# Performance work log

Measured on AMD Instinct MI355X. Metric: run time of the kernel, lower is better.

## Reference

```python
import jax, jax.numpy as jnp
import numpy as np
from jax import lax

B, T, HID = 4, 1024, 1024
H, DK, DV = 8, 128, 128
KCONV = 4
EPS = 1e-6
KEY_DIM = H * DK          # 1024
VAL_DIM = H * DV          # 1024
CONV_DIM = 2 * KEY_DIM + VAL_DIM  # 3072


def setup_inputs() -> dict:
    key = jax.random.key(0)
    ks = jax.random.split(key, 11)
    s = 0.02
    return {
        "hidden_states": jax.random.normal(ks[0], (B, T, HID), jnp.float32),
        "qkv_w": jax.random.normal(ks[1], (CONV_DIM, HID), jnp.float32) * s,
        "z_w": jax.random.normal(ks[2], (VAL_DIM, HID), jnp.float32) * s,
        "b_w": jax.random.normal(ks[3], (H, HID), jnp.float32) * s,
        "a_w": jax.random.normal(ks[4], (H, HID), jnp.float32) * s,
        "conv_w": jax.random.normal(ks[5], (CONV_DIM, 1, KCONV), jnp.float32) * 0.2,
        "dt_bias": jnp.ones((H,), jnp.float32),
        "A_log": jnp.log(jax.random.uniform(ks[6], (H,), jnp.float32, 1e-3, 16.0)),
        "norm_w": jnp.ones((DV,), jnp.float32),
        "out_w": jax.random.normal(ks[7], (HID, VAL_DIM), jnp.float32) * s,
    }


def reference(hidden_states, qkv_w, z_w, b_w, a_w, conv_w, dt_bias, A_log, norm_w, out_w):
    b_, t_, _ = hidden_states.shape

    # qkv projection -> [B, T, CONV_DIM]
    mixed = jnp.einsum("bth,ch->btc", hidden_states, qkv_w)

    # causal depthwise conv1d over time (groups == channels, padding K-1, truncated)
    x = mixed.transpose(0, 2, 1)  # [B, C, T]
    x = lax.conv_general_dilated(
        x, conv_w, window_strides=(1,), padding=[(KCONV - 1, 0)],
        feature_group_count=CONV_DIM,
        dimension_numbers=("NCH", "OIH", "NCH"))
    mixed = x.transpose(0, 2, 1)  # [B, T, C]

    z = jnp.einsum("bth,vh->btv", hidden_states, z_w).reshape(b_, t_, H, DV)
    bb = jnp.einsum("bth,nh->btn", hidden_states, b_w)   # [B,T,H]
    aa = jnp.einsum("bth,nh->btn", hidden_states, a_w)   # [B,T,H]

    q, k, v = jnp.split(mixed, 3, axis=-1)
    q = q.reshape(b_, t_, H, DK)
    k = k.reshape(b_, t_, H, DK)
    v = v.reshape(b_, t_, H, DV)

    beta = jax.nn.sigmoid(bb)                                  # [B,T,H]
    g = -jnp.exp(A_log) * jax.nn.softplus(aa + dt_bias)        # [B,T,H]
    alpha = jnp.exp(g)                                         # per-step decay

    # gated delta rule recurrence, time-major scan
    def step(S, inp):
        q_t, k_t, v_t, beta_t, alpha_t = inp  # [B,H,dk],[B,H,dk],[B,H,dv],[B,H],[B,H]
        S = S * alpha_t[..., None, None]                       # decay state
        kv = jnp.einsum("bhk,bhkv->bhv", k_t, S)              # retrieved memory
        S = S + jnp.einsum("bhk,bhv->bhkv", k_t, (v_t - kv) * beta_t[..., None])
        o_t = jnp.einsum("bhk,bhkv->bhv", q_t, S)
        return S, o_t

    qt = q.transpose(1, 0, 2, 3)
    kt = k.transpose(1, 0, 2, 3)
    vt = v.transpose(1, 0, 2, 3)
    bt = beta.transpose(1, 0, 2)
    at = alpha.transpose(1, 0, 2)
    S0 = jnp.zeros((b_, H, DK, DV), hidden_states.dtype)
    _, o = lax.scan(step, S0, (qt, kt, vt, bt, at))            # o: [T,B,H,dv]
    o = o.transpose(1, 0, 2, 3)                                # [B,T,H,dv]

    # gated RMSNorm: rmsnorm(o) * weight * silu(z)
    var = jnp.mean(jnp.square(o), axis=-1, keepdims=True)
    o = o * lax.rsqrt(var + EPS) * norm_w
    o = o * (z * jax.nn.sigmoid(z))

    out = jnp.einsum("btv,hv->bth", o.reshape(b_, t_, VAL_DIM), out_w)
    return out
```

## Files before the change

### kernel.cpp

```cpp
#include <hip/hip_runtime.h>

#define B_ 4
#define T_ 1024
#define HID_ 1024
#define H_ 8
#define CONV_DIM_ 3072
#define MROWS (B_*T_)

typedef __bf16 bf16x8 __attribute__((ext_vector_type(8)));
typedef float f32x4 __attribute__((ext_vector_type(4)));

#define MFMA16(a,b,c) __builtin_amdgcn_mfma_f32_16x16x32_bf16((a),(b),(c),0,0,0)

static __device__ __forceinline__ unsigned short f2bf(float f) {
  unsigned u = __float_as_uint(f);
  unsigned r = u + 0x7fffu + ((u >> 16) & 1u);
  return (unsigned short)(r >> 16);
}
static __device__ __forceinline__ float bfu2f(unsigned short v) {
  return __uint_as_float(((unsigned)v) << 16);
}
static __device__ __forceinline__ float4 recon4(ushort4 h, ushort4 l) {
  float4 r;
  r.x = bfu2f(h.x) + bfu2f(l.x);
  r.y = bfu2f(h.y) + bfu2f(l.y);
  r.z = bfu2f(h.z) + bfu2f(l.z);
  r.w = bfu2f(h.w) + bfu2f(l.w);
  return r;
}

static __device__ __forceinline__ void gld16(void* lds, const void* g) {
  __builtin_amdgcn_global_load_lds(
      (const __attribute__((address_space(1))) unsigned int*)g,
      (__attribute__((address_space(3))) unsigned int*)lds, 16, 0, 0);
}

__global__ __launch_bounds__(256) void f2bf_kernel(
    const float* __restrict__ src, unsigned short* __restrict__ dst, int n) {
  int i = (blockIdx.x * 256 + threadIdx.x) * 4;
  if (i >= n) return;
  float4 v = *(const float4*)(src + i);
  ushort4 o;
  o.x = f2bf(v.x); o.y = f2bf(v.y); o.z = f2bf(v.z); o.w = f2bf(v.w);
  *(ushort4*)(dst + i) = o;
}

__global__ __launch_bounds__(256) void f2bf_split_kernel(
    const float* __restrict__ src, unsigned short* __restrict__ hi,
    unsigned short* __restrict__ lo, int n) {
  int i = (blockIdx.x * 256 + threadIdx.x) * 4;
  if (i >= n) return;
  float4 v = *(const float4*)(src + i);
  ushort4 h, l;
  h.x = f2bf(v.x); h.y = f2bf(v.y); h.z = f2bf(v.z); h.w = f2bf(v.w);
  l.x = f2bf(v.x - bfu2f(h.x));
  l.y = f2bf(v.y - bfu2f(h.y));
  l.z = f2bf(v.z - bfu2f(h.z));
  l.w = f2bf(v.w - bfu2f(h.w));
  *(ushort4*)(hi + i) = h;
  *(ushort4*)(lo + i) = l;
}

template<int OUT_BF16>
__global__ __launch_bounds__(256) void gemm_mfma_kernel(
    const unsigned short* __restrict__ A, const unsigned short* __restrict__ W,
    void* __restrict__ Cv, int M, int N, int K) {
  __shared__ __align__(16) unsigned short lA[128*32];
  __shared__ __align__(16) unsigned short lB[128*32];
  const int tid  = threadIdx.x;
  const int lane = tid & 63;
  const int wv   = tid >> 6;
  const int wm   = (wv >> 1) * 64;
  const int wn   = (wv & 1) * 64;
  const int m16  = lane & 15;
  const int quad = lane >> 4;
  const int bm = blockIdx.y * 128;
  const int bn = blockIdx.x * 128;

  f32x4 acc[4][4];
  #pragma unroll
  for (int i = 0; i < 4; ++i)
    #pragma unroll
    for (int j = 0; j < 4; ++j)
      acc[i][j] = (f32x4){0.f, 0.f, 0.f, 0.f};

  const int r0 = tid >> 2, c0 = tid & 3;
  const int r1 = r0 + 64;
  const int g0 = (c0 ^ (r0 & 3)) * 8;
  const int g1 = (c0 ^ (r1 & 3)) * 8;
  const unsigned short* Ar0 = A + (size_t)(bm + r0) * K + g0;
  const unsigned short* Ar1 = A + (size_t)(bm + r1) * K + g1;
  const unsigned short* Wr0 = W + (size_t)(bn + r0) * K + g0;
  const unsigned short* Wr1 = W + (size_t)(bn + r1) * K + g1;
  unsigned short* sA0 = &lA[(size_t)tid * 8];
  unsigned short* sA1 = &lA[(size_t)(tid + 256) * 8];
  unsigned short* sB0 = &lB[(size_t)tid * 8];
  unsigned short* sB1 = &lB[(size_t)(tid + 256) * 8];

  int offA[4], offB[4];
  #pragma unroll
  for (int i = 0; i < 4; ++i) {
    int ra = wm + i * 16 + m16;
    offA[i] = ra * 32 + (quad ^ (ra & 3)) * 8;
    int rb = wn + i * 16 + m16;
    offB[i] = rb * 32 + (quad ^ (rb & 3)) * 8;
  }

  for (int k0 = 0; k0 < K; k0 += 32) {
    gld16(sA0, Ar0 + k0);
    gld16(sA1, Ar1 + k0);
    gld16(sB0, Wr0 + k0);
    gld16(sB1, Wr1 + k0);
    __syncthreads();
    bf16x8 af[4], bfr[4];
    #pragma unroll
    for (int i = 0; i < 4; ++i) {
      af[i]  = *(const bf16x8*)&lA[offA[i]];
      bfr[i] = *(const bf16x8*)&lB[offB[i]];
    }
    #pragma unroll
    for (int mi = 0; mi < 4; ++mi)
      #pragma unroll
      for (int ni = 0; ni < 4; ++ni)
        acc[mi][ni] = MFMA16(af[mi], bfr[ni], acc[mi][ni]);
    __syncthreads();
  }

  #pragma unroll
  for (int mi = 0; mi < 4; ++mi) {
    #pragma unroll
    for (int r = 0; r < 4; ++r) {
      size_t row = (size_t)(bm + wm + mi * 16 + quad * 4 + r);
      #pragma unroll
      for (int ni = 0; ni < 4; ++ni) {
        int col = bn + wn + ni * 16 + m16;
        float val = acc[mi][ni][r];
        if (OUT_BF16) ((unsigned short*)Cv)[row * N + col] = f2bf(val);
        else          ((float*)Cv)[row * N + col] = val;
      }
    }
  }
}

__global__ __launch_bounds__(256) void gemm_mfma_split_kernel(
    const unsigned short* __restrict__ Ahi, const unsigned short* __restrict__ Alo,
    const unsigned short* __restrict__ Whi, const unsigned short* __restrict__ Wlo,
    float* __restrict__ C, int M, int N, int K) {
  __shared__ __align__(16) unsigned short lAh[128*32];
  __shared__ __align__(16) unsigned short lAl[128*32];
  __shared__ __align__(16) unsigned short lBh[128*32];
  __shared__ __align__(16) unsigned short lBl[128*32];
  const int tid  = threadIdx.x;
  const int lane = tid & 63;
  const int wv   = tid >> 6;
  const int wm   = (wv >> 1) * 64;
  const int wn   = (wv & 1) * 64;
  const int m16  = lane & 15;
  const int quad = lane >> 4;
  const int bm = blockIdx.y * 128;
  const int bn = blockIdx.x * 128;

  f32x4 acc[4][4];
  #pragma unroll
  for (int i = 0; i < 4; ++i)
    #pragma unroll
    for (int j = 0; j < 4; ++j)
      acc[i][j] = (f32x4){0.f, 0.f, 0.f, 0.f};

  const int r0 = tid >> 2, c0 = tid & 3;
  const int r1 = r0 + 64;
  const int g0 = (c0 ^ (r0 & 3)) * 8;
  const int g1 = (c0 ^ (r1 & 3)) * 8;
  const size_t oA0 = (size_t)(bm + r0) * K + g0;
  const size_t oA1 = (size_t)(bm + r1) * K + g1;
  const size_t oB0 = (size_t)(bn + r0) * K + g0;
  const size_t oB1 = (size_t)(bn + r1) * K + g1;
  const int s0 = tid * 8, s1 = (tid + 256) * 8;

  int offA[4], offB[4];
  #pragma unroll
  for (int i = 0; i < 4; ++i) {
    int ra = wm + i * 16 + m16;
    offA[i] = ra * 32 + (quad ^ (ra & 3)) * 8;
    int rb = wn + i * 16 + m16;
    offB[i] = rb * 32 + (quad ^ (rb & 3)) * 8;
  }

  for (int k0 = 0; k0 < K; k0 += 32) {
    gld16(&lAh[s0], Ahi + oA0 + k0);
    gld16(&lAh[s1], Ahi + oA1 + k0);
    gld16(&lAl[s0], Alo + oA0 + k0);
    gld16(&lAl[s1], Alo + oA1 + k0);
    gld16(&lBh[s0], Whi + oB0 + k0);
    gld16(&lBh[s1], Whi + oB1 + k0);
    gld16(&lBl[s0], Wlo + oB0 + k0);
    gld16(&lBl[s1], Wlo + oB1 + k0);
    __syncthreads();
    bf16x8 afh[4], bfh[4];
    #pragma unroll
    for (int i = 0; i < 4; ++i) {
      afh[i] = *(const bf16x8*)&lAh[offA[i]];
      bfh[i] = *(const bf16x8*)&lBh[offB[i]];
    }
    #pragma unroll
    for (int mi = 0; mi < 4; ++mi)
      #pragma unroll
      for (int ni = 0; ni < 4; ++ni)
        acc[mi][ni] = MFMA16(afh[mi], bfh[ni], acc[mi][ni]);
    {
      bf16x8 bfl[4];
      #pragma unroll
      for (int i = 0; i < 4; ++i) bfl[i] = *(const bf16x8*)&lBl[offB[i]];
      #pragma unroll
      for (int mi = 0; mi < 4; ++mi)
        #pragma unroll
        for (int ni = 0; ni < 4; ++ni)
          acc[mi][ni] = MFMA16(afh[mi], bfl[ni], acc[mi][ni]);
    }
    {
      bf16x8 afl[4];
      #pragma unroll
      for (int i = 0; i < 4; ++i) afl[i] = *(const bf16x8*)&lAl[offA[i]];
      #pragma unroll
      for (int mi = 0; mi < 4; ++mi)
        #pragma unroll
        for (int ni = 0; ni < 4; ++ni)
          acc[mi][ni] = MFMA16(afl[mi], bfh[ni], acc[mi][ni]);
    }
    __syncthreads();
  }

  #pragma unroll
  for (int mi = 0; mi < 4; ++mi) {
    #pragma unroll
    for (int r = 0; r < 4; ++r) {
      size_t row = (size_t)(bm + wm + mi * 16 + quad * 4 + r);
      #pragma unroll
      for (int ni = 0; ni < 4; ++ni)
        C[row * N + bn + wn + ni * 16 + m16] = acc[mi][ni][r];
    }
  }
}

__global__ __launch_bounds__(128) void proj_ba_kernel(
    const float* __restrict__ hs, const float* __restrict__ b_w, const float* __restrict__ a_w,
    const float* __restrict__ dt_bias, const float* __restrict__ A_log,
    float* __restrict__ gout, float* __restrict__ beta) {
  const int bt = blockIdx.x;
  const int b = bt >> 10;
  const int t = bt & 1023;
  const int tid = threadIdx.x;
  const int grp = tid >> 3;
  const int l8 = tid & 7;
  const int h = grp & 7;
  const bool isA = grp >= 8;
  const float* w = (isA ? a_w : b_w) + (size_t)h * HID_;
  const float* x = hs + (size_t)bt * HID_;
  float s = 0.f;
  for (int e = l8*4; e < HID_; e += 32){
    float4 xv = *(const float4*)(x + e);
    float4 wv = *(const float4*)(w + e);
    s = fmaf(xv.x, wv.x, s);
    s = fmaf(xv.y, wv.y, s);
    s = fmaf(xv.z, wv.z, s);
    s = fmaf(xv.w, wv.w, s);
  }
  s += __shfl_xor(s,1); s += __shfl_xor(s,2); s += __shfl_xor(s,4);
  if (l8 == 0) {
    size_t o = ((size_t)(b*H_ + h))*T_ + t;
    if (!isA) {
      beta[o] = 1.f/(1.f+expf(-s));
    } else {
      float xx = s + dt_bias[h];
      float sp = fmaxf(xx,0.f) + log1pf(expf(-fabsf(xx)));
      gout[o] = -expf(A_log[h]) * sp;
    }
  }
}

__global__ __launch_bounds__(256) void conv_route_kernel(
    const float* __restrict__ mixed, const float* __restrict__ conv_w,
    unsigned short* __restrict__ qhi, unsigned short* __restrict__ qlo,
    unsigned short* __restrict__ khi, unsigned short* __restrict__ klo,
    float* __restrict__ vb) {
  const int idx = blockIdx.x*256 + threadIdx.x;
  const int c = idx % CONV_DIM_;
  const int bt4 = idx / CONV_DIM_;
  const int b = bt4 >> 8;
  const int t0 = (bt4 & 255) * 4;
  float w0=conv_w[c*4],w1=conv_w[c*4+1],w2=conv_w[c*4+2],w3=conv_w[c*4+3];
  float x[7];
  #pragma unroll
  for (int j=0;j<7;++j){
    int tt = t0 - 3 + j;
    x[j] = (tt >= 0) ? mixed[((size_t)(b*T_+tt))*CONV_DIM_ + c] : 0.f;
  }
  const int part = c >> 10;
  const int cc = c & 1023;
  const int hh = cc >> 7;
  const int d = cc & 127;
  if (part == 2) {
    size_t base = (((size_t)(b*H_+hh))*T_ + t0)*128 + d;
    #pragma unroll
    for (int i=0;i<4;++i){
      float s = fmaf(w0,x[i],fmaf(w1,x[i+1],fmaf(w2,x[i+2],w3*x[i+3])));
      vb[base + (size_t)i*128] = s;
    }
  } else {
    unsigned short* dh = (part==0) ? qhi : khi;
    unsigned short* dl = (part==0) ? qlo : klo;
    size_t rowb = ((size_t)(b*H_+hh))*T_ + t0;
    #pragma unroll
    for (int i=0;i<4;++i){
      float s = fmaf(w0,x[i],fmaf(w1,x[i+1],fmaf(w2,x[i+2],w3*x[i+3])));
      int tl = (t0 + i) & 7;
      int sw = (((d>>3) ^ tl) << 3) + (d & 7);
      unsigned short hv = f2bf(s);
      dh[(rowb + i)*128 + sw] = hv;
      dl[(rowb + i)*128 + sw] = f2bf(s - bfu2f(hv));
    }
  }
}

__global__ __launch_bounds__(256) void scan_ab_kernel(
    const unsigned short* __restrict__ qhi_g, const unsigned short* __restrict__ qlo_g,
    const unsigned short* __restrict__ khi_g, const unsigned short* __restrict__ klo_g,
    const float* __restrict__ gbuf, const float* __restrict__ bbuf,
    unsigned short* __restrict__ Thi_g, unsigned short* __restrict__ Tlo_g,
    unsigned short* __restrict__ Bhi_g, unsigned short* __restrict__ Blo_g) {
  const int blk = blockIdx.x;
  const int bh = blk >> 4;
  const int ch = blk & 15;
  const int t0 = ch * 64;
  const int tid = threadIdx.x;
  __shared__ float sK[64][132];
  __shared__ float sAA[64][68];
  __shared__ float lL[64];
  __shared__ float bL[64];
  unsigned short* Tho = Thi_g + (size_t)blk*4096;
  unsigned short* Tlo = Tlo_g + (size_t)blk*4096;
  unsigned short* Bho = Bhi_g + (size_t)blk*4096;
  unsigned short* Blo = Blo_g + (size_t)blk*4096;

  #pragma unroll
  for (int i = 0; i < 8; ++i) {
    int f4 = tid + 256*i;
    int row = f4 >> 5, c4 = (f4 & 31) * 4;
    int gr = t0 + row;
    size_t base = ((size_t)bh*1024 + gr)*128;
    int sw = (((c4>>3) ^ (gr&7)) << 3) + (c4 & 7);
    ushort4 h = *(const ushort4*)&khi_g[base + sw];
    ushort4 l = *(const ushort4*)&klo_g[base + sw];
    *(float4*)&sK[row][c4] = recon4(h, l);
  }
  if (tid < 64) {
    float x = gbuf[(size_t)bh*T_ + t0 + tid];
    #pragma unroll
    for (int o = 1; o < 64; o <<= 1) {
      float y = __shfl_up(x, o);
      if (tid >= o) x += y;
    }
    lL[tid] = x;
    bL[tid] = bbuf[(size_t)bh*T_ + t0 + tid];
  }
  __syncthreads();

  const int it = tid >> 4, jt = tid & 15;
  {
    float acc[4][4] = {};
    if (jt <= it) {
      for (int kk = 0; kk < 128; kk += 4) {
        float4 ka[4], kc[4];
        #pragma unroll
        for (int r = 0; r < 4; ++r) {
          ka[r] = *(const float4*)&sK[it*4+r][kk];
          kc[r] = *(const float4*)&sK[jt*4+r][kk];
        }
        #pragma unroll
        for (int a = 0; a < 4; ++a)
          #pragma unroll
          for (int b = 0; b < 4; ++b) {
            acc[a][b] = fmaf(ka[a].x, kc[b].x, acc[a][b]);
            acc[a][b] = fmaf(ka[a].y, kc[b].y, acc[a][b]);
            acc[a][b] = fmaf(ka[a].z, kc[b].z, acc[a][b]);
            acc[a][b] = fmaf(ka[a].w, kc[b].w, acc[a][b]);
          }
      }
    }
    #pragma unroll
    for (int a = 0; a < 4; ++a) {
      int i = it*4 + a;
      float bi = bL[i], li = lL[i];
      #pragma unroll
      for (int b = 0; b < 4; ++b) {
        int j = jt*4 + b;
        sAA[i][j] = (j < i) ? bi * __expf(li - lL[j]) * acc[a][b] : 0.f;
      }
    }
  }
  {
    float acc[4][4] = {};
    if (jt <= it) {
      size_t qbase[4]; int qrx[4];
      #pragma unroll
      for (int r = 0; r < 4; ++r) {
        int gr = t0 + it*4 + r;
        qbase[r] = ((size_t)bh*1024 + gr)*128;
        qrx[r] = gr & 7;
      }
      for (int kk = 0; kk < 128; kk += 4) {
        float4 qa[4], kc[4];
        #pragma unroll
        for (int r = 0; r < 4; ++r) {
          int sw = (((kk>>3) ^ qrx[r]) << 3) + (kk & 7);
          ushort4 h = *(const ushort4*)&qhi_g[qbase[r] + sw];
          ushort4 l = *(const ushort4*)&qlo_g[qbase[r] + sw];
          qa[r] = recon4(h, l);
          kc[r] = *(const float4*)&sK[jt*4+r][kk];
        }
        #pragma unroll
        for (int a = 0; a < 4; ++a)
          #pragma unroll
          for (int b = 0; b < 4; ++b) {
            acc[a][b] = fmaf(qa[a].x, kc[b].x, acc[a][b]);
            acc[a][b] = fmaf(qa[a].y, kc[b].y, acc[a][b]);
            acc[a][b] = fmaf(qa[a].z, kc[b].z, acc[a][b]);
            acc[a][b] = fmaf(qa[a].w, kc[b].w, acc[a][b]);
          }
      }
    }
    #pragma unroll
    for (int a = 0; a < 4; ++a) {
      int i = it*4 + a;
      float li = lL[i];
      #pragma unroll
      for (int b = 0; b < 4; ++b) {
        int j = jt*4 + b;
        float x = (j <= i) ? __expf(li - lL[j]) * acc[a][b] : 0.f;
        unsigned short hv = f2bf(x);
        int sidx = i*64 + (((j>>3) ^ (i&7)) << 3) + (j&7);
        Bho[sidx] = hv;
        Blo[sidx] = f2bf(x - bfu2f(hv));
      }
    }
  }
  __syncthreads();

  {
    const int w = tid >> 6;
    const int ln = tid & 63;
    const int colc = w*16 + (ln & 15);
    const int rr = ln >> 4;
    float rh[16];
    #pragma unroll
    for (int m=0;m<16;++m) rh[m] = (rr + 4*m == colc) ? 1.f : 0.f;
    for (int j = 0; j < 63; ++j) {
      int src = ((j & 3) << 4) | (ln & 15);
      float wj = __shfl(rh[j >> 2], src);
      #pragma unroll
      for (int m=0;m<16;++m)
        rh[m] = fmaf(-sAA[rr + 4*m][j], wj, rh[m]);
    }
    #pragma unroll
    for (int m=0;m<16;++m) {
      int i2 = rr + 4*m;
      float x = rh[m];
      unsigned short hv = f2bf(x);
      int sidx = i2*64 + (((colc>>3) ^ (i2&7)) << 3) + (colc&7);
      Tho[sidx] = hv;
      Tlo[sidx] = f2bf(x - bfu2f(hv));
    }
  }
}

__global__ __launch_bounds__(512) void scan_seq_kernel(
    const unsigned short* __restrict__ khi_g, const unsigned short* __restrict__ klo_g,
    const unsigned short* __restrict__ qhi_g, const unsigned short* __restrict__ qlo_g,
    const float* __restrict__ vb,
    const float* __restrict__ gbuf, const float* __restrict__ bbuf,
    const unsigned short* __restrict__ Thi_g, const unsigned short* __restrict__ Tlo_g,
    const unsigned short* __restrict__ Bhi_g, const unsigned short* __restrict__ Blo_g,
    float* __restrict__ ob) {
  const int bh = blockIdx.x >> 3;
  const int sl = blockIdx.x & 7;
  const int tid = threadIdx.x;
  const int wv = tid >> 6;
  const int lane = tid & 63;
  const int v16 = lane & 15;
  const int quad = lane >> 4;
  const int tb = (wv & 3) * 16;
  const bool isQ = (wv >= 4);
  const int vx = v16 & 7;

  __shared__ __align__(16) unsigned short KhiL[2][64*128];
  __shared__ __align__(16) unsigned short KloL[2][64*128];
  __shared__ __align__(16) unsigned short WTh[16*64],  WTl[16*64];
  __shared__ __align__(16) unsigned short W2Th[16*64], W2Tl[16*64];
  __shared__ __align__(16) unsigned short W3Th[16*64], W3Tl[16*64];
  __shared__ __align__(16) unsigned short S0h[16*128], S0l[16*128];

  const unsigned short* kh  = khi_g + (size_t)bh*131072;
  const unsigned short* klp = klo_g + (size_t)bh*131072;
  const unsigned short* qh  = qhi_g + (size_t)bh*131072;
  const unsigned short* qlp = qlo_g + (size_t)bh*131072;
  const float* vg = vb + (size_t)bh*T_*128 + sl*16;
  const float* gg = gbuf + (size_t)bh*T_;
  const float* beg = bbuf + (size_t)bh*T_;
  float* og = ob + (size_t)bh*T_*128 + sl*16;

  f32x4 sreg = (f32x4){0.f, 0.f, 0.f, 0.f};
  const int kk0 = wv*16 + v16;
  const int k8 = kk0 >> 3, k7 = kk0 & 7;
  const int kq4 = (quad & 1) * 4;
  const int kr8 = (wv*16 + quad*4) >> 3;

  gld16(&KhiL[0][tid*8],        kh + tid*8);
  gld16(&KhiL[0][4096 + tid*8], kh + 4096 + tid*8);
  gld16(&KloL[0][tid*8],        klp + tid*8);
  gld16(&KloL[0][4096 + tid*8], klp + 4096 + tid*8);

  for (int ch = 0; ch < 16; ++ch) {
    const int t0 = ch * 64;
    const int cur = ch & 1;
    __syncthreads();

    if (ch < 15) {
      const size_t co = (size_t)(t0 + 64) * 128;
      gld16(&KhiL[cur^1][tid*8],        kh + co + tid*8);
      gld16(&KhiL[cur^1][4096 + tid*8], kh + co + 4096 + tid*8);
      gld16(&KloL[cur^1][tid*8],        klp + co + tid*8);
      gld16(&KloL[cur^1][4096 + tid*8], klp + co + 4096 + tid*8);
    }

    float gv = gg[t0 + lane];
    #pragma unroll
    for (int o = 1; o < 64; o <<= 1) {
      float y = __shfl_up(gv, o);
      if (lane >= o) gv += y;
    }
    float bv = beg[t0 + lane];

    const int ar = tb + v16;
    const int arx = ar & 7;
    const size_t tbo = ((size_t)(bh*16 + ch)) * 4096;
    bf16x8 tfh0, tfh1, tfl0, tfl1;
    bf16x8 bfh0, bfh1, bfl0, bfl1;
    bf16x8 qfh[4], qfl[4];
    if (!isQ) {
      int a0 = ar*64 + ((quad ^ arx) << 3);
      int a1 = ar*64 + (((4 + quad) ^ arx) << 3);
      tfh0 = *(const bf16x8*)&Thi_g[tbo + a0];
      tfh1 = *(const bf16x8*)&Thi_g[tbo + a1];
      tfl0 = *(const bf16x8*)&Tlo_g[tbo + a0];
      tfl1 = *(const bf16x8*)&Tlo_g[tbo + a1];
    } else {
      int a0 = ar*64 + ((quad ^ arx) << 3);
      int a1 = ar*64 + (((4 + quad) ^ arx) << 3);
      bfh0 = *(const bf16x8*)&Bhi_g[tbo + a0];
      bfh1 = *(const bf16x8*)&Bhi_g[tbo + a1];
      bfl0 = *(const bf16x8*)&Blo_g[tbo + a0];
      bfl1 = *(const bf16x8*)&Blo_g[tbo + a1];
      const size_t qco = (size_t)t0 * 128;
      #pragma unroll
      for (int ks = 0; ks < 4; ++ks) {
        int ao = ar*128 + (((4*ks + quad) ^ arx) << 3);
        qfh[ks] = *(const bf16x8*)&qh[qco + ao];
        qfl[ks] = *(const bf16x8*)&qlp[qco + ao];
      }
    }

    f32x4 facc = (f32x4){0.f,0.f,0.f,0.f};
    if (ch) {
      f32x4 f2 = (f32x4){0.f,0.f,0.f,0.f};
      #pragma unroll
      for (int ks = 0; ks < 4; ++ks) {
        const int u = 4*ks + quad;
        const int bo = v16*128 + ((u ^ vx) << 3);
        bf16x8 bhi = *(const bf16x8*)&S0h[bo];
        bf16x8 blo = *(const bf16x8*)&S0l[bo];
        bf16x8 ahi, alo;
        if (!isQ) {
          const int ao = ar*128 + ((u ^ arx) << 3);
          ahi = *(const bf16x8*)&KhiL[cur][ao];
          alo = *(const bf16x8*)&KloL[cur][ao];
        } else {
          ahi = qfh[ks]; alo = qfl[ks];
        }
        facc = MFMA16(ahi, bhi, facc);
        f2   = MFMA16(ahi, blo, f2);
        f2   = MFMA16(alo, bhi, f2);
      }
      facc[0] += f2[0]; facc[1] += f2[1]; facc[2] += f2[2]; facc[3] += f2[3];
    }
    const int t4 = tb + quad*4;
    const int wo = v16*64 + ((((t4>>3) ^ vx)) << 3) + (t4 & 7);
    f32x4 qacc = facc;
    if (!isQ) {
      float xr[4];
      #pragma unroll
      for (int r = 0; r < 4; ++r) {
        const int t = t4 + r;
        float be = __shfl(bv, t);
        float ga = __expf(__shfl(gv, t));
        float vvv = vg[(size_t)(t0 + t)*128 + v16];
        xr[r] = fmaf(-be*ga, facc[r], be*vvv);
      }
      ushort4 h4, l4;
      h4.x = f2bf(xr[0]); h4.y = f2bf(xr[1]); h4.z = f2bf(xr[2]); h4.w = f2bf(xr[3]);
      l4.x = f2bf(xr[0]-bfu2f(h4.x)); l4.y = f2bf(xr[1]-bfu2f(h4.y));
      l4.z = f2bf(xr[2]-bfu2f(h4.z)); l4.w = f2bf(xr[3]-bfu2f(h4.w));
      *(ushort4*)&WTh[wo] = h4;
      *(ushort4*)&WTl[wo] = l4;
    }
    __syncthreads();

    if (!isQ) {
      f32x4 wa = (f32x4){0.f,0.f,0.f,0.f};
      f32x4 wb = (f32x4){0.f,0.f,0.f,0.f};
      {
        const int b0 = v16*64 + ((quad ^ vx) << 3);
        const int b1 = v16*64 + (((4 + quad) ^ vx) << 3);
        bf16x8 r0h = *(const bf16x8*)&WTh[b0];
        bf16x8 r0l = *(const bf16x8*)&WTl[b0];
        bf16x8 r1h = *(const bf16x8*)&WTh[b1];
        bf16x8 r1l = *(const bf16x8*)&WTl[b1];
        wa = MFMA16(tfh0, r0h, wa);
        wb = MFMA16(tfh0, r0l, wb);
        wb = MFMA16(tfl0, r0h, wb);
        wa = MFMA16(tfh1, r1h, wa);
        wb = MFMA16(tfh1, r1l, wb);
        wb = MFMA16(tfl1, r1h, wb);
      }
      float Le = __shfl(gv, 63);
      float x0 = wa[0]+wb[0], x1 = wa[1]+wb[1], x2 = wa[2]+wb[2], x3 = wa[3]+wb[3];
      ushort4 h4, l4;
      h4.x = f2bf(x0); h4.y = f2bf(x1); h4.z = f2bf(x2); h4.w = f2bf(x3);
      l4.x = f2bf(x0-bfu2f(h4.x)); l4.y = f2bf(x1-bfu2f(h4.y));
      l4.z = f2bf(x2-bfu2f(h4.z)); l4.w = f2bf(x3-bfu2f(h4.w));
      *(ushort4*)&W2Th[wo] = h4;
      *(ushort4*)&W2Tl[wo] = l4;
      float w30 = x0 * __expf(Le - __shfl(gv, t4+0));
      float w31 = x1 * __expf(Le - __shfl(gv, t4+1));
      float w32 = x2 * __expf(Le - __shfl(gv, t4+2));
      float w33 = x3 * __expf(Le - __shfl(gv, t4+3));
      ushort4 h3, l3;
      h3.x = f2bf(w30); h3.y = f2bf(w31); h3.z = f2bf(w32); h3.w = f2bf(w33);
      l3.x = f2bf(w30-bfu2f(h3.x)); l3.y = f2bf(w31-bfu2f(h3.y));
      l3.z = f2bf(w32-bfu2f(h3.z)); l3.w = f2bf(w33-bfu2f(h3.w));
      *(ushort4*)&W3Th[wo] = h3;
      *(ushort4*)&W3Tl[wo] = l3;
    }
    __syncthreads();

    if (isQ) {
      f32x4 oa = (f32x4){0.f,0.f,0.f,0.f};
      f32x4 ob2 = (f32x4){0.f,0.f,0.f,0.f};
      const int b0 = v16*64 + ((quad ^ vx) << 3);
      const int b1 = v16*64 + (((4 + quad) ^ vx) << 3);
      bf16x8 w0h = *(const bf16x8*)&W2Th[b0];
      bf16x8 w0l = *(const bf16x8*)&W2Tl[b0];
      bf16x8 w1h = *(const bf16x8*)&W2Th[b1];
      bf16x8 w1l = *(const bf16x8*)&W2Tl[b1];
      oa  = MFMA16(bfh0, w0h, oa);
      ob2 = MFMA16(bfh0, w0l, ob2);
      ob2 = MFMA16(bfl0, w0h, ob2);
      oa  = MFMA16(bfh1, w1h, oa);
      ob2 = MFMA16(bfh1, w1l, ob2);
      ob2 = MFMA16(bfl1, w1h, ob2);
      #pragma unroll
      for (int r = 0; r < 4; ++r) {
        const int t = t4 + r;
        float ga = __expf(__shfl(gv, t));
        og[(size_t)(t0 + t)*128 + v16] = fmaf(ga, qacc[r], oa[r] + ob2[r]);
      }
    }

    if (ch != 15) {
      float gC = __expf(__shfl(gv, 63));
      sreg[0] *= gC; sreg[1] *= gC; sreg[2] *= gC; sreg[3] *= gC;
      f32x4 s2 = (f32x4){0.f,0.f,0.f,0.f};
      #pragma unroll
      for (int ks = 0; ks < 2; ++ks) {
        const int u = 4*ks + quad;
        const int tbase = u * 8;
        bf16x8 ahi, alo;
        #pragma unroll
        for (int j = 0; j < 8; ++j) {
          const int ad = (tbase + j)*128 + ((k8 ^ j) << 3) + k7;
          ahi[j] = *(const __bf16*)&KhiL[cur][ad];
          alo[j] = *(const __bf16*)&KloL[cur][ad];
        }
        const int bo = v16*64 + ((u ^ vx) << 3);
        bf16x8 bhi = *(const bf16x8*)&W3Th[bo];
        bf16x8 blo = *(const bf16x8*)&W3Tl[bo];
        sreg = MFMA16(ahi, bhi, sreg);
        s2   = MFMA16(ahi, blo, s2);
        s2   = MFMA16(alo, bhi, s2);
      }
      sreg[0] += s2[0]; sreg[1] += s2[1]; sreg[2] += s2[2]; sreg[3] += s2[3];
      const int so = v16*128 + ((kr8 ^ vx) << 3) + kq4;
      ushort4 h4, l4;
      h4.x = f2bf(sreg[0]); h4.y = f2bf(sreg[1]);
      h4.z = f2bf(sreg[2]); h4.w = f2bf(sreg[3]);
      l4.x = f2bf(sreg[0]-bfu2f(h4.x)); l4.y = f2bf(sreg[1]-bfu2f(h4.y));
      l4.z = f2bf(sreg[2]-bfu2f(h4.z)); l4.w = f2bf(sreg[3]-bfu2f(h4.w));
      *(ushort4*)&S0h[so] = h4;
      *(ushort4*)&S0l[so] = l4;
    }
  }
}

__global__ __launch_bounds__(64) void gnorm_kernel(
    const float* __restrict__ ob, const unsigned short* __restrict__ zbb,
    const float* __restrict__ norm_w, unsigned short* __restrict__ og) {
  const int idx = blockIdx.x;
  const int t = idx & 1023;
  const int bh = idx >> 10;
  const int b = bh >> 3;
  const int h = bh & 7;
  const int tid = threadIdx.x;
  const float* o = ob + ((size_t)bh*T_ + t)*128;
  float2 ov = *(const float2*)(o + tid*2);
  float ss = fmaf(ov.x, ov.x, ov.y*ov.y);
  #pragma unroll
  for (int m=1; m<64; m<<=1) ss += __shfl_xor(ss, m);
  float inv = rsqrtf(ss*(1.f/128.f) + 1e-6f);
  size_t zoff = ((size_t)(b*T_+t))*1024 + (size_t)h*128 + tid*2;
  ushort2 zv = *(const ushort2*)(zbb + zoff);
  float z0 = bfu2f(zv.x), z1 = bfu2f(zv.y);
  float n0 = norm_w[tid*2], n1 = norm_w[tid*2+1];
  float r0 = ov.x*inv*n0 * z0/(1.f+expf(-z0));
  float r1 = ov.y*inv*n1 * z1/(1.f+expf(-z1));
  ushort2 ot;
  ot.x = f2bf(r0); ot.y = f2bf(r1);
  *(ushort2*)(og + zoff) = ot;
}

extern "C" void kernel_launch(void* const* d_in, const int* in_sizes, int n_in,
                              void* d_out, int out_size, void* d_ws, size_t ws_size,
                              hipStream_t stream) {
  const float* hs     = (const float*)d_in[0];
  const float* qkv_w  = (const float*)d_in[1];
  const float* z_w    = (const float*)d_in[2];
  const float* b_w    = (const float*)d_in[3];
  const float* a_w    = (const float*)d_in[4];
  const float* conv_w = (const float*)d_in[5];
  const float* dt_bias= (const float*)d_in[6];
  const float* A_log  = (const float*)d_in[7];
  const float* norm_w = (const float*)d_in[8];
  const float* out_w  = (const float*)d_in[9];
  float* out = (float*)d_out;

  char* wsp = (char*)d_ws;
  size_t off = 0;
  auto give = [&](size_t bytes)->char*{
    char* p = wsp + off; off += (bytes + 255) & ~(size_t)255; return p;
  };
  float* mixed  = (float*)give((size_t)MROWS*CONV_DIM_*4);
  unsigned short* zbuf = (unsigned short*)give((size_t)MROWS*1024*2);
  unsigned short* outw_bf = (unsigned short*)give((size_t)HID_*1024*2);
  float* qb    = (float*)give((size_t)32*T_*128*4);
  float* kb    = (float*)give((size_t)32*T_*128*4);
  float* vb    = (float*)give((size_t)32*T_*128*4);
  float* gbuf  = (float*)give((size_t)32*T_*4);
  float* beta  = (float*)give((size_t)32*T_*4);
  unsigned short* hs_hi = (unsigned short*)kb;
  unsigned short* hs_lo = (unsigned short*)kb + (size_t)MROWS*HID_;
  unsigned short* wc_hi = (unsigned short*)vb;
  unsigned short* wc_lo = (unsigned short*)vb + (size_t)CONV_DIM_*HID_;
  unsigned short* wz_bf = (unsigned short*)qb;
  unsigned short* qhi = (unsigned short*)qb;
  unsigned short* qlo = qhi + (size_t)32*T_*128;
  unsigned short* khi = (unsigned short*)kb;
  unsigned short* klo = khi + (size_t)32*T_*128;
  float* ob = mixed;
  unsigned short* og = (unsigned short*)(mixed + (size_t)4*1024*1024);
  unsigned short* Thi_g = (unsigned short*)(mixed + (size_t)6*1024*1024);
  unsigned short* Tlo_g = Thi_g + (size_t)512*4096;
  unsigned short* Bhi_g = Tlo_g + (size_t)512*4096;
  unsigned short* Blo_g = Bhi_g + (size_t)512*4096;

  f2bf_split_kernel<<<dim3(MROWS*HID_/1024), 256, 0, stream>>>(hs, hs_hi, hs_lo, MROWS*HID_);
  f2bf_split_kernel<<<dim3(CONV_DIM_*HID_/1024), 256, 0, stream>>>(qkv_w, wc_hi, wc_lo, CONV_DIM_*HID_);
  f2bf_kernel<<<dim3(1024*HID_/1024), 256, 0, stream>>>(z_w, wz_bf, 1024*HID_);
  f2bf_kernel<<<dim3(1024*HID_/1024), 256, 0, stream>>>(out_w, outw_bf, 1024*HID_);

  gemm_mfma_split_kernel<<<dim3(CONV_DIM_/128, MROWS/128), 256, 0, stream>>>(
      hs_hi, hs_lo, wc_hi, wc_lo, mixed, MROWS, CONV_DIM_, HID_);
  gemm_mfma_kernel<1><<<dim3(1024/128, MROWS/128), 256, 0, stream>>>(
      hs_hi, wz_bf, zbuf, MROWS, 1024, HID_);
  proj_ba_kernel<<<dim3(MROWS), dim3(128), 0, stream>>>(hs, b_w, a_w, dt_bias, A_log, gbuf, beta);
  conv_route_kernel<<<dim3((B_*256*CONV_DIM_)/256), dim3(256), 0, stream>>>(
      mixed, conv_w, qhi, qlo, khi, klo, vb);
  scan_ab_kernel<<<dim3(512), dim3(256), 0, stream>>>(
      qhi, qlo, khi, klo, gbuf, beta, Thi_g, Tlo_g, Bhi_g, Blo_g);
  scan_seq_kernel<<<dim3(256), dim3(512), 0, stream>>>(
      khi, klo, qhi, qlo, vb, gbuf, beta, Thi_g, Tlo_g, Bhi_g, Blo_g, ob);
  gnorm_kernel<<<dim3(32*T_), dim3(64), 0, stream>>>(ob, zbuf, norm_w, og);
  gemm_mfma_kernel<0><<<dim3(1024/128, MROWS/128), 256, 0, stream>>>(og, outw_bf, out, MROWS, 1024, HID_);
}
```

Baseline: 403.6 us.

## Fuse causal conv into QKV GEMM epilogue and fold hs bf16 split into proj_ba

```diff
diff --git a/kernel.cpp b/kernel.cpp
--- a/kernel.cpp
+++ b/kernel.cpp
@@ -142,14 +142,20 @@
   }
 }
 
-__global__ __launch_bounds__(256) void gemm_mfma_split_kernel(
+__global__ __launch_bounds__(256) void gemm_split_conv_kernel(
     const unsigned short* __restrict__ Ahi, const unsigned short* __restrict__ Alo,
     const unsigned short* __restrict__ Whi, const unsigned short* __restrict__ Wlo,
-    float* __restrict__ C, int M, int N, int K) {
-  __shared__ __align__(16) unsigned short lAh[128*32];
-  __shared__ __align__(16) unsigned short lAl[128*32];
-  __shared__ __align__(16) unsigned short lBh[128*32];
-  __shared__ __align__(16) unsigned short lBl[128*32];
+    const float* __restrict__ conv_w,
+    unsigned short* __restrict__ qhi, unsigned short* __restrict__ qlo,
+    unsigned short* __restrict__ khi, unsigned short* __restrict__ klo,
+    float* __restrict__ vb) {
+  __shared__ __align__(16) unsigned char ldsraw[128*132*4];
+  unsigned short* lAh = (unsigned short*)ldsraw;
+  unsigned short* lAl = lAh + 128*32;
+  unsigned short* lBh = lAl + 128*32;
+  unsigned short* lBl = lBh + 128*32;
+  float* smX = (float*)ldsraw;
+
   const int tid  = threadIdx.x;
   const int lane = tid & 63;
   const int wv   = tid >> 6;
@@ -171,10 +177,10 @@
   const int r1 = r0 + 64;
   const int g0 = (c0 ^ (r0 & 3)) * 8;
   const int g1 = (c0 ^ (r1 & 3)) * 8;
-  const size_t oA0 = (size_t)(bm + r0) * K + g0;
-  const size_t oA1 = (size_t)(bm + r1) * K + g1;
-  const size_t oB0 = (size_t)(bn + r0) * K + g0;
-  const size_t oB1 = (size_t)(bn + r1) * K + g1;
+  const size_t oA0 = (size_t)(bm + r0) * 1024 + g0;
+  const size_t oA1 = (size_t)(bm + r1) * 1024 + g1;
+  const size_t oB0 = (size_t)(bn + r0) * 1024 + g0;
+  const size_t oB1 = (size_t)(bn + r1) * 1024 + g1;
   const int s0 = tid * 8, s1 = (tid + 256) * 8;
 
   int offA[4], offB[4];
@@ -186,7 +192,7 @@
     offB[i] = rb * 32 + (quad ^ (rb & 3)) * 8;
   }
 
-  for (int k0 = 0; k0 < K; k0 += 32) {
+  for (int k0 = 0; k0 < 1024; k0 += 32) {
     gld16(&lAh[s0], Ahi + oA0 + k0);
     gld16(&lAh[s1], Ahi + oA1 + k0);
     gld16(&lAl[s0], Alo + oA0 + k0);
@@ -234,10 +240,118 @@
   for (int mi = 0; mi < 4; ++mi) {
     #pragma unroll
     for (int r = 0; r < 4; ++r) {
-      size_t row = (size_t)(bm + wm + mi * 16 + quad * 4 + r);
+      int row = wm + mi * 16 + quad * 4 + r;
       #pragma unroll
       for (int ni = 0; ni < 4; ++ni)
-        C[row * N + bn + wn + ni * 16 + m16] = acc[mi][ni][r];
+        smX[row * 132 + wn + ni * 16 + m16] = acc[mi][ni][r];
+    }
+  }
+  __syncthreads();
+
+  {
+    const int c  = tid & 127;
+    const int rh = tid >> 7;
+    const int cg = bn + c;
+    const int part = cg >> 10;
+    const int hh = (cg & 1023) >> 7;
+    const int b = bm >> 10;
+    const int tloc0 = bm & 1023;
+    float4 w4 = *(const float4*)(conv_w + cg * 4);
+    size_t rowb = ((size_t)(b * H_ + hh)) * T_;
+    const int tb0 = rh * 64;
+    float x0 = (tb0 >= 3) ? smX[(tb0-3)*132 + c] : 0.f;
+    float x1 = (tb0 >= 2) ? smX[(tb0-2)*132 + c] : 0.f;
+    float x2 = (tb0 >= 1) ? smX[(tb0-1)*132 + c] : 0.f;
+    unsigned short* dh = (part == 0) ? qhi : khi;
+    unsigned short* dl = (part == 0) ? qlo : klo;
+    for (int tt = 0; tt < 64; ++tt) {
+      const int t = tb0 + tt;
+      float x3 = smX[t*132 + c];
+      float s = fmaf(w4.x, x0, fmaf(w4.y, x1, fmaf(w4.z, x2, w4.w * x3)));
+      x0 = x1; x1 = x2; x2 = x3;
+      const int tg = tloc0 + t;
+      if (part == 2) {
+        vb[(rowb + tg) * 128 + c] = s;
+      } else {
+        int sw = (((c >> 3) ^ (tg & 7)) << 3) + (c & 7);
+        unsigned short hv = f2bf(s);
+        dh[(rowb + tg) * 128 + sw] = hv;
+        dl[(rowb + tg) * 128 + sw] = f2bf(s - bfu2f(hv));
+      }
+    }
+  }
+}
+
+__global__ __launch_bounds__(256) void conv_fix_kernel(
+    const unsigned short* __restrict__ Ahi, const unsigned short* __restrict__ Alo,
+    const unsigned short* __restrict__ Whi, const unsigned short* __restrict__ Wlo,
+    const float* __restrict__ conv_w,
+    unsigned short* __restrict__ qhi, unsigned short* __restrict__ qlo,
+    unsigned short* __restrict__ khi, unsigned short* __restrict__ klo,
+    float* __restrict__ vb) {
+  const int bi = blockIdx.x / 24;
+  const int cb = blockIdx.x % 24;
+  const int bm = bi * 128, n0 = cb * 128;
+  const int b = bm >> 10, tloc = bm & 1023;
+  const int tid = threadIdx.x;
+  __shared__ float sA[6][1032];
+  __shared__ float sM[6][132];
+
+  for (int z = tid; z < 6 * 256; z += 256) {
+    int j = z >> 8, c4 = (z & 255) * 4;
+    int tr = tloc - 3 + j;
+    float4 v = {0.f, 0.f, 0.f, 0.f};
+    if (tr >= 0) {
+      size_t o = ((size_t)(b * 1024 + tr)) * 1024 + c4;
+      v = recon4(*(const ushort4*)(Ahi + o), *(const ushort4*)(Alo + o));
+    }
+    *(float4*)&sA[j][c4] = v;
+  }
+  __syncthreads();
+
+  {
+    const int c = tid & 127, rg = tid >> 7;
+    const int j0 = rg * 3;
+    float a0 = 0.f, a1 = 0.f, a2 = 0.f;
+    const unsigned short* wh = Whi + (size_t)(n0 + c) * 1024;
+    const unsigned short* wl = Wlo + (size_t)(n0 + c) * 1024;
+    for (int k = 0; k < 1024; k += 4) {
+      float4 wv = recon4(*(const ushort4*)(wh + k), *(const ushort4*)(wl + k));
+      float4 m0 = *(const float4*)&sA[j0 + 0][k];
+      float4 m1 = *(const float4*)&sA[j0 + 1][k];
+      float4 m2 = *(const float4*)&sA[j0 + 2][k];
+      a0 = fmaf(wv.x, m0.x, fmaf(wv.y, m0.y, fmaf(wv.z, m0.z, fmaf(wv.w, m0.w, a0))));
+      a1 = fmaf(wv.x, m1.x, fmaf(wv.y, m1.y, fmaf(wv.z, m1.z, fmaf(wv.w, m1.w, a1))));
+      a2 = fmaf(wv.x, m2.x, fmaf(wv.y, m2.y, fmaf(wv.z, m2.z, fmaf(wv.w, m2.w, a2))));
+    }
+    sM[j0 + 0][c] = a0;
+    sM[j0 + 1][c] = a1;
+    sM[j0 + 2][c] = a2;
+  }
+  __syncthreads();
+
+  if (tid < 128) {
+    const int c = tid;
+    const int cg = n0 + c;
+    const int part = cg >> 10;
+    const int hh = (cg & 1023) >> 7;
+    float4 w4 = *(const float4*)(conv_w + cg * 4);
+    size_t rowb = ((size_t)(b * H_ + hh)) * T_;
+    unsigned short* dh = (part == 0) ? qhi : khi;
+    unsigned short* dl = (part == 0) ? qlo : klo;
+    #pragma unroll
+    for (int jo = 0; jo < 3; ++jo) {
+      float s = fmaf(w4.x, sM[jo][c], fmaf(w4.y, sM[jo+1][c],
+                fmaf(w4.z, sM[jo+2][c], w4.w * sM[jo+3][c])));
+      const int tg = tloc + jo;
+      if (part == 2) {
+        vb[(rowb + tg) * 128 + c] = s;
+      } else {
+        int sw = (((c >> 3) ^ (tg & 7)) << 3) + (c & 7);
+        unsigned short hv = f2bf(s);
+        dh[(rowb + tg) * 128 + sw] = hv;
+        dl[(rowb + tg) * 128 + sw] = f2bf(s - bfu2f(hv));
+      }
     }
   }
 }
@@ -245,7 +359,8 @@
 __global__ __launch_bounds__(128) void proj_ba_kernel(
     const float* __restrict__ hs, const float* __restrict__ b_w, const float* __restrict__ a_w,
     const float* __restrict__ dt_bias, const float* __restrict__ A_log,
-    float* __restrict__ gout, float* __restrict__ beta) {
+    float* __restrict__ gout, float* __restrict__ beta,
+    unsigned short* __restrict__ hs_hi, unsigned short* __restrict__ hs_lo) {
   const int bt = blockIdx.x;
   const int b = bt >> 10;
   const int t = bt & 1023;
@@ -256,6 +371,9 @@
   const bool isA = grp >= 8;
   const float* w = (isA ? a_w : b_w) + (size_t)h * HID_;
   const float* x = hs + (size_t)bt * HID_;
+  unsigned short* hho = hs_hi + (size_t)bt * HID_;
+  unsigned short* hlo = hs_lo + (size_t)bt * HID_;
+  const bool emit = (grp == 0);
   float s = 0.f;
   for (int e = l8*4; e < HID_; e += 32){
     float4 xv = *(const float4*)(x + e);
@@ -264,6 +382,16 @@
     s = fmaf(xv.y, wv.y, s);
     s = fmaf(xv.z, wv.z, s);
     s = fmaf(xv.w, wv.w, s);
+    if (emit) {
+      ushort4 hq, lq;
+      hq.x = f2bf(xv.x); hq.y = f2bf(xv.y); hq.z = f2bf(xv.z); hq.w = f2bf(xv.w);
+      lq.x = f2bf(xv.x - bfu2f(hq.x));
+      lq.y = f2bf(xv.y - bfu2f(hq.y));
+      lq.z = f2bf(xv.z - bfu2f(hq.z));
+      lq.w = f2bf(xv.w - bfu2f(hq.w));
+      *(ushort4*)(hho + e) = hq;
+      *(ushort4*)(hlo + e) = lq;
+    }
   }
   s += __shfl_xor(s,1); s += __shfl_xor(s,2); s += __shfl_xor(s,4);
   if (l8 == 0) {
@@ -274,50 +402,6 @@
       float xx = s + dt_bias[h];
       float sp = fmaxf(xx,0.f) + log1pf(expf(-fabsf(xx)));
       gout[o] = -expf(A_log[h]) * sp;
-    }
-  }
-}
-
-__global__ __launch_bounds__(256) void conv_route_kernel(
-    const float* __restrict__ mixed, const float* __restrict__ conv_w,
-    unsigned short* __restrict__ qhi, unsigned short* __restrict__ qlo,
-    unsigned short* __restrict__ khi, unsigned short* __restrict__ klo,
-    float* __restrict__ vb) {
-  const int idx = blockIdx.x*256 + threadIdx.x;
-  const int c = idx % CONV_DIM_;
-  const int bt4 = idx / CONV_DIM_;
-  const int b = bt4 >> 8;
-  const int t0 = (bt4 & 255) * 4;
-  float w0=conv_w[c*4],w1=conv_w[c*4+1],w2=conv_w[c*4+2],w3=conv_w[c*4+3];
-  float x[7];
-  #pragma unroll
-  for (int j=0;j<7;++j){
-    int tt = t0 - 3 + j;
-    x[j] = (tt >= 0) ? mixed[((size_t)(b*T_+tt))*CONV_DIM_ + c] : 0.f;
-  }
-  const int part = c >> 10;
-  const int cc = c & 1023;
-  const int hh = cc >> 7;
-  const int d = cc & 127;
-  if (part == 2) {
-    size_t base = (((size_t)(b*H_+hh))*T_ + t0)*128 + d;
-    #pragma unroll
-    for (int i=0;i<4;++i){
-      float s = fmaf(w0,x[i],fmaf(w1,x[i+1],fmaf(w2,x[i+2],w3*x[i+3])));
-      vb[base + (size_t)i*128] = s;
-    }
-  } else {
-    unsigned short* dh = (part==0) ? qhi : khi;
-    unsigned short* dl = (part==0) ? qlo : klo;
-    size_t rowb = ((size_t)(b*H_+hh))*T_ + t0;
-    #pragma unroll
-    for (int i=0;i<4;++i){
-      float s = fmaf(w0,x[i],fmaf(w1,x[i+1],fmaf(w2,x[i+2],w3*x[i+3])));
-      int tl = (t0 + i) & 7;
-      int sw = (((d>>3) ^ tl) << 3) + (d & 7);
-      unsigned short hv = f2bf(s);
-      dh[(rowb + i)*128 + sw] = hv;
-      dl[(rowb + i)*128 + sw] = f2bf(s - bfu2f(hv));
     }
   }
 }
@@ -756,46 +840,47 @@
   auto give = [&](size_t bytes)->char*{
     char* p = wsp + off; off += (bytes + 255) & ~(size_t)255; return p;
   };
-  float* mixed  = (float*)give((size_t)MROWS*CONV_DIM_*4);
+  char* big    = give((size_t)MROWS*CONV_DIM_*4);
   unsigned short* zbuf = (unsigned short*)give((size_t)MROWS*1024*2);
   unsigned short* outw_bf = (unsigned short*)give((size_t)HID_*1024*2);
-  float* qb    = (float*)give((size_t)32*T_*128*4);
-  float* kb    = (float*)give((size_t)32*T_*128*4);
-  float* vb    = (float*)give((size_t)32*T_*128*4);
+  char* bufA   = give((size_t)32*T_*128*4);
+  char* bufB   = give((size_t)32*T_*128*4);
+  char* bufC   = give((size_t)32*T_*128*4);
   float* gbuf  = (float*)give((size_t)32*T_*4);
   float* beta  = (float*)give((size_t)32*T_*4);
-  unsigned short* hs_hi = (unsigned short*)kb;
-  unsigned short* hs_lo = (unsigned short*)kb + (size_t)MROWS*HID_;
-  unsigned short* wc_hi = (unsigned short*)vb;
-  unsigned short* wc_lo = (unsigned short*)vb + (size_t)CONV_DIM_*HID_;
-  unsigned short* wz_bf = (unsigned short*)qb;
-  unsigned short* qhi = (unsigned short*)qb;
-  unsigned short* qlo = qhi + (size_t)32*T_*128;
-  unsigned short* khi = (unsigned short*)kb;
-  unsigned short* klo = khi + (size_t)32*T_*128;
-  float* ob = mixed;
-  unsigned short* og = (unsigned short*)(mixed + (size_t)4*1024*1024);
-  unsigned short* Thi_g = (unsigned short*)(mixed + (size_t)6*1024*1024);
+
+  unsigned short* khi = (unsigned short*)big;
+  unsigned short* klo = khi + (size_t)4*1024*1024;
+  unsigned short* qhi = klo + (size_t)4*1024*1024;
+  unsigned short* qlo = qhi + (size_t)4*1024*1024;
+  float* vdat = (float*)(qlo + (size_t)4*1024*1024);
+  unsigned short* wz_bf = (unsigned short*)bufA;
+  unsigned short* Blo_g = (unsigned short*)bufA + (size_t)1024*1024;
+  unsigned short* og    = (unsigned short*)bufA + (size_t)3*1024*1024;
+  unsigned short* hs_hi = (unsigned short*)bufB;
+  unsigned short* hs_lo = hs_hi + (size_t)MROWS*HID_;
+  unsigned short* Thi_g = (unsigned short*)bufB;
   unsigned short* Tlo_g = Thi_g + (size_t)512*4096;
   unsigned short* Bhi_g = Tlo_g + (size_t)512*4096;
-  unsigned short* Blo_g = Bhi_g + (size_t)512*4096;
-
-  f2bf_split_kernel<<<dim3(MROWS*HID_/1024), 256, 0, stream>>>(hs, hs_hi, hs_lo, MROWS*HID_);
+  unsigned short* wc_hi = (unsigned short*)bufC;
+  unsigned short* wc_lo = wc_hi + (size_t)CONV_DIM_*HID_;
+  float* ob = (float*)bufC;
+
   f2bf_split_kernel<<<dim3(CONV_DIM_*HID_/1024), 256, 0, stream>>>(qkv_w, wc_hi, wc_lo, CONV_DIM_*HID_);
   f2bf_kernel<<<dim3(1024*HID_/1024), 256, 0, stream>>>(z_w, wz_bf, 1024*HID_);
   f2bf_kernel<<<dim3(1024*HID_/1024), 256, 0, stream>>>(out_w, outw_bf, 1024*HID_);
-
-  gemm_mfma_split_kernel<<<dim3(CONV_DIM_/128, MROWS/128), 256, 0, stream>>>(
-      hs_hi, hs_lo, wc_hi, wc_lo, mixed, MROWS, CONV_DIM_, HID_);
+  proj_ba_kernel<<<dim3(MROWS), dim3(128), 0, stream>>>(
+      hs, b_w, a_w, dt_bias, A_log, gbuf, beta, hs_hi, hs_lo);
   gemm_mfma_kernel<1><<<dim3(1024/128, MROWS/128), 256, 0, stream>>>(
       hs_hi, wz_bf, zbuf, MROWS, 1024, HID_);
-  proj_ba_kernel<<<dim3(MROWS), dim3(128), 0, stream>>>(hs, b_w, a_w, dt_bias, A_log, gbuf, beta);
-  conv_route_kernel<<<dim3((B_*256*CONV_DIM_)/256), dim3(256), 0, stream>>>(
-      mixed, conv_w, qhi, qlo, khi, klo, vb);
+  gemm_split_conv_kernel<<<dim3(CONV_DIM_/128, MROWS/128), 256, 0, stream>>>(
+      hs_hi, hs_lo, wc_hi, wc_lo, conv_w, qhi, qlo, khi, klo, vdat);
+  conv_fix_kernel<<<dim3(32*24), 256, 0, stream>>>(
+      hs_hi, hs_lo, wc_hi, wc_lo, conv_w, qhi, qlo, khi, klo, vdat);
   scan_ab_kernel<<<dim3(512), dim3(256), 0, stream>>>(
       qhi, qlo, khi, klo, gbuf, beta, Thi_g, Tlo_g, Bhi_g, Blo_g);
   scan_seq_kernel<<<dim3(256), dim3(512), 0, stream>>>(
-      khi, klo, qhi, qlo, vb, gbuf, beta, Thi_g, Tlo_g, Bhi_g, Blo_g, ob);
+      khi, klo, qhi, qlo, vdat, gbuf, beta, Thi_g, Tlo_g, Bhi_g, Blo_g, ob);
   gnorm_kernel<<<dim3(32*T_), dim3(64), 0, stream>>>(ob, zbuf, norm_w, og);
   gemm_mfma_kernel<0><<<dim3(1024/128, MROWS/128), 256, 0, stream>>>(og, outw_bf, out, MROWS, 1024, HID_);
 }
```

Result: slower. 554.0 us (+37.3%).
